# Optimization experiments

Measured on AMD Instinct MI355X. Metric: run time of the kernel, lower is better.

Reference implementation:

```python
import jax, jax.numpy as jnp
import numpy as np

B, T, H = 16, 512, 768
S = 32            # gold spans per example
L = 50            # max_span_len -> candidate ends per span
NT = 3            # num_types
HS = 4 * H        # span repr size


def setup_inputs() -> dict:
    key = jax.random.key(0)
    ks = jax.random.split(key, 8)
    h = jax.random.normal(ks[0], (B, T, H), dtype=jnp.float32)
    attention_mask = jnp.ones((B, T), dtype=jnp.int32)
    starts = jax.random.randint(ks[1], (B, S), 1, 400).astype(jnp.int32)
    lens = jax.random.randint(ks[2], (B, S), 0, L).astype(jnp.int32)
    ends = starts + lens                      # <= 448 < last_tok=510
    types = jax.random.randint(ks[3], (B, S), 0, NT).astype(jnp.int32)
    W1 = jax.random.normal(ks[4], (HS, HS), dtype=jnp.float32) * (1.0 / np.sqrt(HS))
    b1 = jnp.zeros((HS,), dtype=jnp.float32)
    w_score = jax.random.normal(ks[5], (HS,), dtype=jnp.float32) * (1.0 / np.sqrt(HS))
    b_score = jnp.zeros((1,), dtype=jnp.float32)
    W_type = jax.random.normal(ks[6], (HS, NT), dtype=jnp.float32) * (1.0 / np.sqrt(HS))
    b_type = jnp.zeros((NT,), dtype=jnp.float32)
    return {"h": h, "attention_mask": attention_mask, "span_starts": starts,
            "span_ends": ends, "span_types": types, "W1": W1, "b1": b1,
            "w_score": w_score, "b_score": b_score, "W_type": W_type, "b_type": b_type}


def _span_loss(h, attention_mask, span_starts, span_ends, span_types,
               W1, b1, w_score, b_score, W_type, b_type, type_loss_weight=1.0):
    cls = h[:, 0]                                              # [B,H]
    # prefix sums for O(1) segment means: pre[b,t] = sum h[b,0:t]
    pre = jnp.concatenate([jnp.zeros((B, 1, H), h.dtype), jnp.cumsum(h, axis=1)], axis=1)

    valid_len = attention_mask.sum(axis=1)                     # [B]
    last_tok = jnp.maximum(1, valid_len - 2)                   # [B]

    s = span_starts                                            # [B,S]
    e_gold = span_ends
    gold_idx = e_gold - s                                      # [B,S]
    lt = last_tok[:, None]
    span_valid = (s >= 1) & (s <= lt) & (e_gold >= s) & (e_gold <= lt) & (gold_idx < L)

    e_max = jnp.minimum(s + L - 1, lt)                         # [B,S]
    p = s[..., None] + jnp.arange(L, dtype=s.dtype)            # [B,S,L] candidate ends
    cand_valid = p <= e_max[..., None]

    sc = jnp.clip(s, 0, T - 1)
    pc = jnp.clip(p, 0, T - 1)
    bi2 = jnp.arange(B)[:, None]
    bi3 = jnp.arange(B)[:, None, None]

    h_start = h[bi2, sc]                                       # [B,S,H]
    h_end = h[bi3, pc]                                         # [B,S,L,H]
    seg_len = jnp.maximum(p - s[..., None] + 1, 1).astype(h.dtype)
    h_mean = (pre[bi3, pc + 1] - pre[bi2, sc][:, :, None]) / seg_len[..., None]

    repr_ = jnp.concatenate([
        jnp.broadcast_to(h_start[:, :, None], (B, S, L, H)),
        h_end,
        h_mean,
        jnp.broadcast_to(cls[:, None, None], (B, S, L, H)),
    ], axis=-1)                                                # [B,S,L,4H]

    h1 = jax.nn.gelu(jnp.einsum('bslh,hd->bsld', repr_, W1) + b1, approximate=False)
    scores = jnp.einsum('bsld,d->bsl', h1, w_score) + b_score[0]      # [B,S,L]
    type_logits = jnp.einsum('bsld,dk->bslk', h1, W_type) + b_type    # [B,S,L,NT]

    # end-index CE over valid candidate ends
    masked = jnp.where(cand_valid, scores, jnp.float32(-1e9))
    logp_end = jax.nn.log_softmax(masked, axis=-1)             # [B,S,L]
    gi = jnp.clip(gold_idx, 0, L - 1)
    end_loss = -jnp.take_along_axis(logp_end, gi[..., None], axis=-1)[..., 0]  # [B,S]

    # type CE at the gold end index
    tl_gold = jnp.take_along_axis(type_logits, gi[..., None, None], axis=2)[:, :, 0]  # [B,S,NT]
    logp_t = jax.nn.log_softmax(tl_gold, axis=-1)
    tg = jnp.clip(span_types, 0, NT - 1)
    type_loss = -jnp.take_along_axis(logp_t, tg[..., None], axis=-1)[..., 0]  # [B,S]

    vmask = span_valid.astype(h.dtype)
    n_seg = vmask.sum()
    denom = jnp.maximum(n_seg, 1.0)
    loss_end = jnp.where(n_seg > 0, (end_loss * vmask).sum() / denom, 0.0)
    loss_type = jnp.where(n_seg > 0, (type_loss * vmask).sum() / denom, 0.0)
    return loss_end + type_loss_weight * loss_type


def reference(h, attention_mask, span_starts, span_ends, span_types,
              W1, b1, w_score, b_score, W_type, b_type):
    return _span_loss(h, attention_mask, span_starts, span_ends, span_types,
                      W1, b1, w_score, b_score, W_type, b_type)
```

## Files before the change

kernel.cpp:

```cpp
#include <hip/hip_runtime.h>
#include <hip/hip_bf16.h>
#include <math.h>

#define B_ 16
#define T_ 512
#define H_ 768
#define S_ 32
#define L_ 50
#define NT_ 3
#define HS_ 3072
#define CH_ 32
#define CT_ 16

#define XROWS 8192
#define YBASE 8192
#define GBASE 16512
#define XYROWS 16400
#define AROWS 17152

typedef __attribute__((ext_vector_type(8))) short short8;
typedef __attribute__((ext_vector_type(16))) float float16v;

__device__ __forceinline__ unsigned short f2bf(float f) {
    __hip_bfloat16 b = __float2bfloat16(f);
    return *(unsigned short*)&b;
}
__device__ __forceinline__ float bf2f(unsigned short u) {
    union { unsigned int i; float f; } v; v.i = ((unsigned int)u) << 16; return v.f;
}
__device__ __forceinline__ void load_lds16(const void* g, void* l) {
    __builtin_amdgcn_global_load_lds((__attribute__((address_space(1))) void*)g,
                                     (__attribute__((address_space(3))) void*)l, 16, 0, 0);
}
__device__ __forceinline__ ushort4 pack4(float4 v) {
    ushort4 o; o.x = f2bf(v.x); o.y = f2bf(v.y); o.z = f2bf(v.z); o.w = f2bf(v.w);
    return o;
}

__device__ __forceinline__ float gelu_exact(float v) {
    float a = fabsf(v) * 0.70710678118654752f;
    float t = __builtin_amdgcn_rcpf(fmaf(a, 0.47047f, 1.0f));
    float poly = t * fmaf(t, fmaf(t, 0.7478556f, -0.0958798f), 0.3480242f);
    float e = __builtin_amdgcn_exp2f(a * a * -1.4426950408889634f);
    float erfa = fmaf(-poly, e, 1.0f);
    float erfv = copysignf(erfa, v);
    return 0.5f * v * (1.0f + erfv);
}

__global__ __launch_bounds__(256) void cumsum_pass1(const float4* __restrict__ h4,
                                                    float4* __restrict__ partial) {
    int idx = blockIdx.x * 256 + threadIdx.x;
    int hd4 = idx % 192; int t = idx / 192; int ch = t % CH_; int b = t / CH_;
    const float4* hp = h4 + ((size_t)b * T_ + ch * CT_) * 192 + hd4;
    float4 acc = {0.f, 0.f, 0.f, 0.f};
#pragma unroll
    for (int tt = 0; tt < CT_; tt++) {
        float4 v = hp[(size_t)tt * 192];
        acc.x += v.x; acc.y += v.y; acc.z += v.z; acc.w += v.w;
    }
    partial[idx] = acc;
}

__global__ __launch_bounds__(256) void cumsum_pass3(const float4* __restrict__ h4,
                                                    const float4* __restrict__ partial,
                                                    ushort4* __restrict__ Ab4) {
    int idx = blockIdx.x * 256 + threadIdx.x;
    int hd4 = idx % 192; int t = idx / 192; int ch = t % CH_; int b = t / CH_;
    float4 acc = {0.f, 0.f, 0.f, 0.f};
#pragma unroll
    for (int c = 0; c < CH_; c++) {
        if (c < ch) {
            float4 v = partial[((size_t)b * CH_ + c) * 192 + hd4];
            acc.x += v.x; acc.y += v.y; acc.z += v.z; acc.w += v.w;
        }
    }
    int row0 = b * T_ + ch * CT_;
    const float4* hp = h4 + (size_t)row0 * 192 + hd4;
    ushort4* hb = Ab4 + (size_t)row0 * 192 + hd4;
    ushort4* pp = Ab4 + ((size_t)(YBASE + b * (T_ + 1) + ch * CT_ + 1)) * 192 + hd4;
    if (ch == 0) {
        ushort4 z = {0, 0, 0, 0};
        Ab4[((size_t)(YBASE + b * (T_ + 1))) * 192 + hd4] = z;
    }
#pragma unroll
    for (int tt = 0; tt < CT_; tt++) {
        float4 hv = hp[(size_t)tt * 192];
        hb[(size_t)tt * 192] = pack4(hv);
        acc.x += hv.x; acc.y += hv.y; acc.z += hv.z; acc.w += hv.w;
        pp[(size_t)tt * 192] = pack4(acc);
    }
}

__global__ void gather_kernel(const float* __restrict__ h,
                              const int* __restrict__ starts,
                              __hip_bfloat16* __restrict__ Ab) {
    int r = blockIdx.x;
    int src_row;
    if (r < B_ * S_) {
        int b = r / S_;
        int sv = starts[r];
        int sc = min(max(sv, 0), T_ - 1);
        src_row = b * T_ + sc;
    } else {
        int b = r - B_ * S_;
        src_row = b * T_;
    }
    __hip_bfloat16* dst = Ab + (size_t)(GBASE + r) * H_;
    for (int j = threadIdx.x; j < H_; j += 256)
        dst[j] = __float2bfloat16(h[(size_t)src_row * H_ + j]);
}

__global__ __launch_bounds__(256) void transpose_w(const float* __restrict__ W1,
                                                   __hip_bfloat16* __restrict__ Wt) {
    __shared__ float tile[64][65];
    int n0 = blockIdx.x * 64, k0 = blockIdx.y * 64;
    int c = threadIdx.x & 63, r0 = threadIdx.x >> 6;
#pragma unroll
    for (int i = 0; i < 16; i++) {
        int r = r0 + i * 4;
        tile[r][c] = W1[(size_t)(k0 + r) * HS_ + n0 + c];
    }
    __syncthreads();
    int p = k0 / H_, kl = k0 % H_;
    __hip_bfloat16* out = Wt + (size_t)p * HS_ * H_;
#pragma unroll
    for (int i = 0; i < 16; i++) {
        int r = r0 + i * 4;
        out[(size_t)(n0 + r) * H_ + kl + c] = __float2bfloat16(tile[c][r]);
    }
}

__global__ __launch_bounds__(256) void mfma_gemm(const __hip_bfloat16* __restrict__ Ab,
                                                 const __hip_bfloat16* __restrict__ Wt,
                                                 __hip_bfloat16* __restrict__ XY,
                                                 float* __restrict__ ST,
                                                 float* __restrict__ CC) {
    constexpr int K = H_;
    __shared__ __hip_bfloat16 As[2 * 128 * 32];
    __shared__ __hip_bfloat16 Bs[2 * 128 * 32];
    int tid = threadIdx.x;
    int wave = tid >> 6, lane = tid & 63;
    int n0 = blockIdx.x * 128, m0 = blockIdx.y * 128;
    int wm = (wave & 1) * 64, wn = (wave >> 1) * 64;

    const __hip_bfloat16* Bt;
    if (m0 < XROWS)            Bt = Wt + (size_t)1 * HS_ * H_;
    else if (m0 < GBASE)       Bt = Wt + (size_t)2 * HS_ * H_;
    else if (m0 < GBASE + 512) Bt = Wt;
    else                       Bt = Wt + (size_t)3 * HS_ * H_;

    float16v acc[2][2] = {};

    int l31 = lane & 31, lh = lane >> 5;

    for (int k0 = 0; k0 < K; k0 += 64) {
        __syncthreads();
#pragma unroll
        for (int i = 0; i < 4; i++) {
            int cid = i * 256 + wave * 64 + lane;
            int hh = cid >> 9, row = (cid >> 2) & 127, pc = cid & 3;
            int lc = pc ^ ((row >> 1) & 3);
            size_t go = (size_t)row * K + k0 + hh * 32 + lc * 8;
            load_lds16(Ab + (size_t)m0 * K + go,
                       (char*)As + (size_t)(i * 256 + wave * 64) * 16);
            load_lds16(Bt + (size_t)n0 * K + go,
                       (char*)Bs + (size_t)(i * 256 + wave * 64) * 16);
        }
        __syncthreads();

        const short* Asp = (const short*)As;
        const short* Bsp = (const short*)Bs;
#pragma unroll
        for (int kk = 0; kk < 4; kk++) {
            int hh = kk >> 1;
            int lc = 2 * (kk & 1) + lh;
            short8 af[2], bf[2];
#pragma unroll
            for (int mi = 0; mi < 2; mi++) {
                int row = wm + mi * 32 + l31;
                int pc = lc ^ ((row >> 1) & 3);
                af[mi] = *(const short8*)&Asp[(hh * 512 + row * 4 + pc) * 8];
            }
#pragma unroll
            for (int ni = 0; ni < 2; ni++) {
                int row = wn + ni * 32 + l31;
                int pc = lc ^ ((row >> 1) & 3);
                bf[ni] = *(const short8*)&Bsp[(hh * 512 + row * 4 + pc) * 8];
            }
#pragma unroll
            for (int mi = 0; mi < 2; mi++)
#pragma unroll
                for (int ni = 0; ni < 2; ni++)
                    acc[mi][ni] = __builtin_amdgcn_mfma_f32_32x32x16_bf16(
                        af[mi], bf[ni], acc[mi][ni], 0, 0, 0);
        }
    }

#pragma unroll
    for (int mi = 0; mi < 2; mi++) {
#pragma unroll
        for (int ni = 0; ni < 2; ni++) {
            int n = n0 + wn + ni * 32 + l31;
#pragma unroll
            for (int r = 0; r < 16; r++) {
                int m = m0 + wm + mi * 32 + (r & 3) + 8 * (r >> 2) + 4 * lh;
                float v = acc[mi][ni][r];
                if (m < XYROWS) {
                    XY[(size_t)m * HS_ + n] = __float2bfloat16(v);
                } else if (m >= GBASE && m < GBASE + 512) {
                    ST[(size_t)(m - GBASE) * HS_ + n] = v;
                } else if (m >= GBASE + 512 && m < GBASE + 528) {
                    CC[(size_t)(m - GBASE - 512) * HS_ + n] = v;
                }
            }
        }
    }
}

__global__ __launch_bounds__(256) void c0_kernel(const float4* __restrict__ ST,
                                                 const float4* __restrict__ CC,
                                                 const float4* __restrict__ b1,
                                                 ushort4* __restrict__ c0b) {
    int i = blockIdx.x * 256 + threadIdx.x;
    int row = i / (HS_ / 4);
    int b = row >> 5;
    int c4 = i % (HS_ / 4);
    float4 s = ST[i], c = CC[b * (HS_ / 4) + c4], bb = b1[c4];
    float4 v = {s.x + c.x + bb.x, s.y + c.y + bb.y, s.z + c.z + bb.z, s.w + c.w + bb.w};
    c0b[i] = pack4(v);
}

__global__ __launch_bounds__(256) void combine_kernel(
    const unsigned short* __restrict__ c0, const __hip_bfloat16* __restrict__ XY,
    const float* __restrict__ w_score, const float* __restrict__ b_score,
    const float* __restrict__ W_type,
    const int* __restrict__ starts, const int* __restrict__ ends,
    float* __restrict__ scores, float* __restrict__ tgold) {
    int bs = blockIdx.x;
    int b = bs >> 5;
    int wave = threadIdx.x >> 6, lane = threadIdx.x & 63;
    int l = blockIdx.y * 4 + wave;
    if (l >= L_) return;
    int sv = starts[bs], ev = ends[bs];
    int gi = min(max(ev - sv, 0), L_ - 1);
    int sc = min(max(sv, 0), T_ - 1);
    int p = sv + l;
    int pc = min(max(p, 0), T_ - 1);
    float invlen = 1.0f / (float)(l + 1);
    bool isg = (l == gi);

    const unsigned short* Xr = (const unsigned short*)(XY + (size_t)(b * T_ + pc) * HS_);
    const unsigned short* Yp = (const unsigned short*)(XY + (size_t)(YBASE + b * (T_ + 1) + pc + 1) * HS_);
    const unsigned short* Ys = (const unsigned short*)(XY + (size_t)(YBASE + b * (T_ + 1) + sc) * HS_);
    const unsigned short* c0r = c0 + (size_t)bs * HS_;

    float local = 0.f, t0 = 0.f, t1 = 0.f, t2 = 0.f;
#pragma unroll
    for (int j = 0; j < 6; j++) {
        int d = j * 512 + lane * 8;
        short8 xv = *(const short8*)(Xr + d);
        short8 yv = *(const short8*)(Yp + d);
        short8 sv8 = *(const short8*)(Ys + d);
        short8 cv8 = *(const short8*)(c0r + d);
        float4 wa = *(const float4*)(w_score + d);
        float4 wb = *(const float4*)(w_score + d + 4);
        float wv[8] = {wa.x, wa.y, wa.z, wa.w, wb.x, wb.y, wb.z, wb.w};
#pragma unroll
        for (int q = 0; q < 8; q++) {
            float x = bf2f(((const unsigned short*)&xv)[q]);
            float y = bf2f(((const unsigned short*)&yv)[q]);
            float ys = bf2f(((const unsigned short*)&sv8)[q]);
            float cv = bf2f(((const unsigned short*)&cv8)[q]);
            float v = fmaf(y - ys, invlen, cv) + x;
            float g = gelu_exact(v);
            local = fmaf(g, wv[q], local);
            if (isg) {
                t0 = fmaf(g, W_type[(d + q) * NT_ + 0], t0);
                t1 = fmaf(g, W_type[(d + q) * NT_ + 1], t1);
                t2 = fmaf(g, W_type[(d + q) * NT_ + 2], t2);
            }
        }
    }
#pragma unroll
    for (int off = 32; off >= 1; off >>= 1) local += __shfl_down(local, off);
    if (lane == 0) scores[(size_t)bs * L_ + l] = local + b_score[0];
    if (isg) {
#pragma unroll
        for (int off = 32; off >= 1; off >>= 1) {
            t0 += __shfl_down(t0, off);
            t1 += __shfl_down(t1, off);
            t2 += __shfl_down(t2, off);
        }
        if (lane == 0) {
            tgold[bs * NT_ + 0] = t0;
            tgold[bs * NT_ + 1] = t1;
            tgold[bs * NT_ + 2] = t2;
        }
    }
}

__global__ __launch_bounds__(512) void loss_kernel(
    const float* __restrict__ scores, const float* __restrict__ tgold,
    const int* __restrict__ mask, const int* __restrict__ starts,
    const int* __restrict__ ends, const int* __restrict__ types,
    const float* __restrict__ b_type, float* __restrict__ out) {
    __shared__ int svl[B_];
    __shared__ float r[3][8];
    int tid = threadIdx.x;
    int b = tid / S_;
    if (tid < B_) svl[tid] = 0;
    __syncthreads();
    {
        int part = 0;
        const int* mp = mask + tid * 16;
#pragma unroll
        for (int i = 0; i < 16; i++) part += mp[i];
        atomicAdd(&svl[tid / (T_ / 16)], part);
    }
    __syncthreads();
    int vl = svl[b];
    int lt = max(1, vl - 2);
    int sv = starts[tid], ev = ends[tid];
    int gold = ev - sv;
    bool valid = (sv >= 1) && (sv <= lt) && (ev >= sv) && (ev <= lt) && (gold < L_);
    int emax = min(sv + L_ - 1, lt);
    const float* sp = scores + (size_t)tid * L_;
    float m = -1e30f;
    for (int l = 0; l < L_; l++) {
        float v = (sv + l <= emax) ? sp[l] : -1e9f;
        m = fmaxf(m, v);
    }
    float sum = 0.f;
    for (int l = 0; l < L_; l++) {
        float v = (sv + l <= emax) ? sp[l] : -1e9f;
        sum += expf(v - m);
    }
    int gi = min(max(gold, 0), L_ - 1);
    float vg = (sv + gi <= emax) ? sp[gi] : -1e9f;
    float end_loss = (m + logf(sum)) - vg;

    float t0 = tgold[tid * 3 + 0] + b_type[0];
    float t1 = tgold[tid * 3 + 1] + b_type[1];
    float t2 = tgold[tid * 3 + 2] + b_type[2];
    float tm = fmaxf(t0, fmaxf(t1, t2));
    float tsum = expf(t0 - tm) + expf(t1 - tm) + expf(t2 - tm);
    int tg = min(max(types[tid], 0), NT_ - 1);
    float tv = (tg == 0) ? t0 : ((tg == 1) ? t1 : t2);
    float type_loss = (tm + logf(tsum)) - tv;

    float ve = valid ? end_loss : 0.f;
    float vt = valid ? type_loss : 0.f;
    float vc = valid ? 1.f : 0.f;
    for (int off = 32; off >= 1; off >>= 1) {
        ve += __shfl_down(ve, off);
        vt += __shfl_down(vt, off);
        vc += __shfl_down(vc, off);
    }
    if ((tid & 63) == 0) {
        int w = tid >> 6;
        r[0][w] = ve; r[1][w] = vt; r[2][w] = vc;
    }
    __syncthreads();
    if (tid == 0) {
        float se = 0, st = 0, n = 0;
        for (int w = 0; w < 8; w++) { se += r[0][w]; st += r[1][w]; n += r[2][w]; }
        float denom = fmaxf(n, 1.f);
        out[0] = (n > 0.f) ? (se / denom + st / denom) : 0.f;
    }
}

extern "C" void kernel_launch(void* const* d_in, const int* in_sizes, int n_in,
                              void* d_out, int out_size, void* d_ws, size_t ws_size,
                              hipStream_t stream) {
    const float* h       = (const float*)d_in[0];
    const int*   mask    = (const int*)d_in[1];
    const int*   starts  = (const int*)d_in[2];
    const int*   ends    = (const int*)d_in[3];
    const int*   types   = (const int*)d_in[4];
    const float* W1      = (const float*)d_in[5];
    const float* b1      = (const float*)d_in[6];
    const float* w_score = (const float*)d_in[7];
    const float* b_score = (const float*)d_in[8];
    const float* W_type  = (const float*)d_in[9];
    const float* b_type  = (const float*)d_in[10];
    float* out = (float*)d_out;

    char* ws = (char*)d_ws;
    size_t off = 0;
    __hip_bfloat16* Ab = (__hip_bfloat16*)(ws + off); off += (size_t)AROWS * H_ * 2;
    __hip_bfloat16* XY = (__hip_bfloat16*)(ws + off); off += (size_t)XYROWS * HS_ * 2;
    __hip_bfloat16* Wt = (__hip_bfloat16*)(ws + off); off += (size_t)4 * HS_ * H_ * 2;
    float* ST     = (float*)(ws + off);               off += (size_t)512 * HS_ * 4;
    float* CC     = (float*)(ws + off);               off += (size_t)16 * HS_ * 4;
    unsigned short* c0b = (unsigned short*)(ws + off); off += (size_t)512 * HS_ * 2;
    float* scores = (float*)(ws + off);               off += (size_t)B_ * S_ * L_ * 4;
    float* tgold  = (float*)(ws + off);               off += (size_t)B_ * S_ * NT_ * 4;
    float4* partial = (float4*)XY;

    hipLaunchKernelGGL(cumsum_pass1, dim3(B_ * CH_ * 192 / 256), dim3(256), 0, stream,
                       (const float4*)h, partial);
    hipLaunchKernelGGL(cumsum_pass3, dim3(B_ * CH_ * 192 / 256), dim3(256), 0, stream,
                       (const float4*)h, partial, (ushort4*)Ab);
    hipLaunchKernelGGL(gather_kernel, dim3(B_ * S_ + B_), dim3(256), 0, stream, h, starts, Ab);
    hipLaunchKernelGGL(transpose_w, dim3(48, 48), dim3(256), 0, stream, W1, Wt);

    hipLaunchKernelGGL(mfma_gemm, dim3(24, AROWS / 128), dim3(256), 0, stream,
                       Ab, Wt, XY, ST, CC);
    hipLaunchKernelGGL(c0_kernel, dim3(512 * HS_ / 4 / 256), dim3(256), 0, stream,
                       (const float4*)ST, (const float4*)CC, (const float4*)b1,
                       (ushort4*)c0b);
    hipLaunchKernelGGL(combine_kernel, dim3(B_ * S_, 13), dim3(256), 0, stream,
                       c0b, XY, w_score, b_score, W_type, starts, ends, scores, tgold);
    hipLaunchKernelGGL(loss_kernel, dim3(1), dim3(512), 0, stream,
                       scores, tgold, mask, starts, ends, types, b_type, out);
}
```

Before: 343.0 us.

## Double-buffer GEMM LDS staging and loop combine over candidate ends per wave

The MFMA GEMM now keeps two LDS buffers and issues the global-to-LDS loads for the next K tile before computing on the current one, dropping one barrier per iteration and aiming to hide load latency behind MFMA work. The combine kernel shrinks its grid from 13 to 2 blocks in y, and each wave loops over several candidate end positions, reusing the start-row and c0 pointers. The cost is double the LDS footprint per GEMM block, which may reduce occupancy, and a much smaller combine grid, which exposes less parallelism.

```diff
diff --git a/kernel.cpp b/kernel.cpp
--- a/kernel.cpp
+++ b/kernel.cpp
@@ -136,8 +136,9 @@
                                                  float* __restrict__ ST,
                                                  float* __restrict__ CC) {
     constexpr int K = H_;
-    __shared__ __hip_bfloat16 As[2 * 128 * 32];
-    __shared__ __hip_bfloat16 Bs[2 * 128 * 32];
+    constexpr int NIT = K / 64;
+    __shared__ __hip_bfloat16 As[2][2 * 128 * 32];
+    __shared__ __hip_bfloat16 Bs[2][2 * 128 * 32];
     int tid = threadIdx.x;
     int wave = tid >> 6, lane = tid & 63;
     int n0 = blockIdx.x * 128, m0 = blockIdx.y * 128;
@@ -149,27 +150,41 @@
     else if (m0 < GBASE + 512) Bt = Wt;
     else                       Bt = Wt + (size_t)3 * HS_ * H_;
 
+    const __hip_bfloat16* Arow = Ab + (size_t)m0 * K;
+    const __hip_bfloat16* Brow = Bt + (size_t)n0 * K;
+
     float16v acc[2][2] = {};
-
     int l31 = lane & 31, lh = lane >> 5;
 
-    for (int k0 = 0; k0 < K; k0 += 64) {
+    int srow[4], sgo_pc[4], soff[4];
+#pragma unroll
+    for (int i = 0; i < 4; i++) {
+        int cid = i * 256 + wave * 64 + lane;
+        int hh = cid >> 9, row = (cid >> 2) & 127, pc = cid & 3;
+        int lc = pc ^ ((row >> 1) & 3);
+        srow[i] = row;
+        sgo_pc[i] = hh * 32 + lc * 8;
+        soff[i] = (i * 256 + wave * 64) * 16;
+    }
+
+#define STAGE(buf, k0)                                                        \
+    {                                                                         \
+        _Pragma("unroll")                                                     \
+        for (int i = 0; i < 4; i++) {                                         \
+            size_t go = (size_t)srow[i] * K + (k0) + sgo_pc[i];               \
+            load_lds16(Arow + go, (char*)As[buf] + soff[i]);                  \
+            load_lds16(Brow + go, (char*)Bs[buf] + soff[i]);                  \
+        }                                                                     \
+    }
+
+    STAGE(0, 0)
+    int cur = 0;
+    for (int it = 0; it < NIT; it++) {
         __syncthreads();
-#pragma unroll
-        for (int i = 0; i < 4; i++) {
-            int cid = i * 256 + wave * 64 + lane;
-            int hh = cid >> 9, row = (cid >> 2) & 127, pc = cid & 3;
-            int lc = pc ^ ((row >> 1) & 3);
-            size_t go = (size_t)row * K + k0 + hh * 32 + lc * 8;
-            load_lds16(Ab + (size_t)m0 * K + go,
-                       (char*)As + (size_t)(i * 256 + wave * 64) * 16);
-            load_lds16(Bt + (size_t)n0 * K + go,
-                       (char*)Bs + (size_t)(i * 256 + wave * 64) * 16);
-        }
-        __syncthreads();
-
-        const short* Asp = (const short*)As;
-        const short* Bsp = (const short*)Bs;
+        if (it + 1 < NIT) STAGE(cur ^ 1, (it + 1) * 64)
+
+        const short* Asp = (const short*)As[cur];
+        const short* Bsp = (const short*)Bs[cur];
 #pragma unroll
         for (int kk = 0; kk < 4; kk++) {
             int hh = kk >> 1;
@@ -194,7 +209,9 @@
                     acc[mi][ni] = __builtin_amdgcn_mfma_f32_32x32x16_bf16(
                         af[mi], bf[ni], acc[mi][ni], 0, 0, 0);
         }
-    }
+        cur ^= 1;
+    }
+#undef STAGE
 
 #pragma unroll
     for (int mi = 0; mi < 2; mi++) {
@@ -239,52 +256,61 @@
     int bs = blockIdx.x;
     int b = bs >> 5;
     int wave = threadIdx.x >> 6, lane = threadIdx.x & 63;
-    int l = blockIdx.y * 4 + wave;
-    if (l >= L_) return;
+    int widx = blockIdx.y * 4 + wave;
     int sv = starts[bs], ev = ends[bs];
     int gi = min(max(ev - sv, 0), L_ - 1);
     int sc = min(max(sv, 0), T_ - 1);
-    int p = sv + l;
-    int pc = min(max(p, 0), T_ - 1);
-    float invlen = 1.0f / (float)(l + 1);
-    bool isg = (l == gi);
-
-    const unsigned short* Xr = (const unsigned short*)(XY + (size_t)(b * T_ + pc) * HS_);
-    const unsigned short* Yp = (const unsigned short*)(XY + (size_t)(YBASE + b * (T_ + 1) + pc + 1) * HS_);
-    const unsigned short* Ys = (const unsigned short*)(XY + (size_t)(YBASE + b * (T_ + 1) + sc) * HS_);
+
+    const unsigned short* Ysr = (const unsigned short*)(XY + (size_t)(YBASE + b * (T_ + 1) + sc) * HS_);
     const unsigned short* c0r = c0 + (size_t)bs * HS_;
-
-    float local = 0.f, t0 = 0.f, t1 = 0.f, t2 = 0.f;
-#pragma unroll
-    for (int j = 0; j < 6; j++) {
-        int d = j * 512 + lane * 8;
-        short8 xv = *(const short8*)(Xr + d);
-        short8 yv = *(const short8*)(Yp + d);
-        short8 sv8 = *(const short8*)(Ys + d);
-        short8 cv8 = *(const short8*)(c0r + d);
-        float4 wa = *(const float4*)(w_score + d);
-        float4 wb = *(const float4*)(w_score + d + 4);
-        float wv[8] = {wa.x, wa.y, wa.z, wa.w, wb.x, wb.y, wb.z, wb.w};
-#pragma unroll
-        for (int q = 0; q < 8; q++) {
-            float x = bf2f(((const unsigned short*)&xv)[q]);
-            float y = bf2f(((const unsigned short*)&yv)[q]);
-            float ys = bf2f(((const unsigned short*)&sv8)[q]);
-            float cv = bf2f(((const unsigned short*)&cv8)[q]);
-            float v = fmaf(y - ys, invlen, cv) + x;
-            float g = gelu_exact(v);
-            local = fmaf(g, wv[q], local);
-            if (isg) {
-                t0 = fmaf(g, W_type[(d + q) * NT_ + 0], t0);
-                t1 = fmaf(g, W_type[(d + q) * NT_ + 1], t1);
-                t2 = fmaf(g, W_type[(d + q) * NT_ + 2], t2);
+    float bs0 = b_score[0];
+
+    float t0 = 0.f, t1 = 0.f, t2 = 0.f;
+    bool hadg = false;
+
+    for (int l = widx; l < L_; l += 8) {
+        int p = sv + l;
+        int pc = min(max(p, 0), T_ - 1);
+        float invlen = 1.0f / (float)(l + 1);
+        bool isg = (l == gi);
+        hadg |= isg;
+
+        const unsigned short* Xr = (const unsigned short*)(XY + (size_t)(b * T_ + pc) * HS_);
+        const unsigned short* Yp = (const unsigned short*)(XY + (size_t)(YBASE + b * (T_ + 1) + pc + 1) * HS_);
+
+        float local = 0.f;
+#pragma unroll
+        for (int j = 0; j < 6; j++) {
+            int d = j * 512 + lane * 8;
+            short8 xv = *(const short8*)(Xr + d);
+            short8 yv = *(const short8*)(Yp + d);
+            short8 sv8 = *(const short8*)(Ysr + d);
+            short8 cv8 = *(const short8*)(c0r + d);
+            float4 wa = *(const float4*)(w_score + d);
+            float4 wb = *(const float4*)(w_score + d + 4);
+            float wv[8] = {wa.x, wa.y, wa.z, wa.w, wb.x, wb.y, wb.z, wb.w};
+#pragma unroll
+            for (int q = 0; q < 8; q++) {
+                float x = bf2f(((const unsigned short*)&xv)[q]);
+                float y = bf2f(((const unsigned short*)&yv)[q]);
+                float ys = bf2f(((const unsigned short*)&sv8)[q]);
+                float cv = bf2f(((const unsigned short*)&cv8)[q]);
+                float v = fmaf(y - ys, invlen, cv) + x;
+                float g = gelu_exact(v);
+                local = fmaf(g, wv[q], local);
+                if (isg) {
+                    t0 = fmaf(g, W_type[(d + q) * NT_ + 0], t0);
+                    t1 = fmaf(g, W_type[(d + q) * NT_ + 1], t1);
+                    t2 = fmaf(g, W_type[(d + q) * NT_ + 2], t2);
+                }
             }
         }
-    }
-#pragma unroll
-    for (int off = 32; off >= 1; off >>= 1) local += __shfl_down(local, off);
-    if (lane == 0) scores[(size_t)bs * L_ + l] = local + b_score[0];
-    if (isg) {
+#pragma unroll
+        for (int off = 32; off >= 1; off >>= 1) local += __shfl_down(local, off);
+        if (lane == 0) scores[(size_t)bs * L_ + l] = local + bs0;
+    }
+
+    if (hadg) {
 #pragma unroll
         for (int off = 32; off >= 1; off >>= 1) {
             t0 += __shfl_down(t0, off);
@@ -409,7 +435,7 @@
     hipLaunchKernelGGL(c0_kernel, dim3(512 * HS_ / 4 / 256), dim3(256), 0, stream,
                        (const float4*)ST, (const float4*)CC, (const float4*)b1,
                        (ushort4*)c0b);
-    hipLaunchKernelGGL(combine_kernel, dim3(B_ * S_, 13), dim3(256), 0, stream,
+    hipLaunchKernelGGL(combine_kernel, dim3(B_ * S_, 2), dim3(256), 0, stream,
                        c0b, XY, w_score, b_score, W_type, starts, ends, scores, tgold);
     hipLaunchKernelGGL(loss_kernel, dim3(1), dim3(512), 0, stream,
                        scores, tgold, mask, starts, ends, types, b_type, out);
```

New measurement: 437.3 us. 1.27x slower.
